# Kernel optimization log

Measured on AMD Instinct MI355X. Metric: run time of the kernel, lower is better.

Reference implementation:

```python
import jax, jax.numpy as jnp
import numpy as np

DIM = 256
N = 8192

def setup_inputs() -> dict:
    key = jax.random.key(0)
    kx, kq, kk, kv = jax.random.split(key, 4)
    X = jax.random.normal(kx, (N, DIM), dtype=jnp.float32)
    # nn.Linear weights are [out, in]; xavier-uniform-like scale via normal/sqrt(dim)
    Wq = jax.random.normal(kq, (DIM, DIM), dtype=jnp.float32) / np.sqrt(DIM)
    Wk = jax.random.normal(kk, (DIM, DIM), dtype=jnp.float32) / np.sqrt(DIM)
    Wv = jax.random.normal(kv, (DIM, DIM), dtype=jnp.float32) / np.sqrt(DIM)
    return {"X": X, "Wq": Wq, "Wk": Wk, "Wv": Wv}

def reference(X, Wq, Wk, Wv):
    # nn.Linear(no bias): y = X @ W.T
    Q = X @ Wq.T  # [N, D]
    K = X @ Wk.T
    V = X @ Wv.T
    scores = (Q @ K.T) / jnp.sqrt(jnp.asarray(DIM, dtype=X.dtype))  # [N, N]
    softed = jax.nn.softmax(scores, axis=-1)
    return softed @ V  # [N, D]
```

## Files before the change

### kernel.cpp

```cpp
#include <hip/hip_runtime.h>
#include <math.h>

#define N 8192
#define D 256
#define QBLK 128
#define KBLK 32

typedef float f32x4 __attribute__((ext_vector_type(4)));
typedef float f32x16 __attribute__((ext_vector_type(16)));
typedef short bf16x8 __attribute__((ext_vector_type(8)));

#define MFMA16(a, b, c) __builtin_amdgcn_mfma_f32_16x16x32_bf16((a), (b), (c), 0, 0, 0)
#define MFMA32(a, b, c) __builtin_amdgcn_mfma_f32_32x32x16_bf16((a), (b), (c), 0, 0, 0)
#define BAR() __builtin_amdgcn_s_barrier()
#define CFENCE() asm volatile("" ::: "memory")

__device__ __forceinline__ unsigned short f2b(float f) {
    unsigned u = __builtin_bit_cast(unsigned, f);
    u = u + 0x7fffu + ((u >> 16) & 1u);
    return (unsigned short)(u >> 16);
}
__device__ __forceinline__ unsigned pk2(float a, float b) {
    return (unsigned)f2b(a) | ((unsigned)f2b(b) << 16);
}
__device__ __forceinline__ unsigned cvtpk(float a, float b) {
    unsigned r;
    asm("v_cvt_pk_bf16_f32 %0, %1, %2" : "=v"(r) : "v"(a), "v"(b));
    return r;
}
__device__ __forceinline__ float b2f(short s) {
    unsigned x = ((unsigned)(unsigned short)s) << 16;
    return __builtin_bit_cast(float, x);
}

__global__ __launch_bounds__(256) void proj_mfma(
    const float* __restrict__ X, const float* __restrict__ Wq,
    const float* __restrict__ Wk, const float* __restrict__ Wv,
    unsigned short* __restrict__ Qb, unsigned short* __restrict__ Kb,
    unsigned short* __restrict__ Vt)
{
    __shared__ char Wl[32768];
    const int z = blockIdx.z;
    const float* W = (z == 0) ? Wq : (z == 1) ? Wk : Wv;
    const int r0 = blockIdx.x * 64;
    const int c0 = blockIdx.y * 64;
    const int t = threadIdx.x, w = t >> 6, l = t & 63;
    const int lo = l & 15, hi = l >> 4;

    #pragma unroll
    for (int i = 0; i < 16; ++i) {
        int e4 = t + i * 256;
        int col = e4 >> 6, kk4 = e4 & 63;
        float4 f = *(const float4*)&W[(size_t)(c0 + col) * D + kk4 * 4];
        unsigned long long v = (unsigned long long)pk2(f.x, f.y)
                             | ((unsigned long long)pk2(f.z, f.w) << 32);
        *(unsigned long long*)(Wl + col * 512 + ((kk4 * 8) ^ ((col & 7) << 4))) = v;
    }
    __syncthreads();

    bf16x8 xf[8];
    {
        const float* xr = X + (size_t)(r0 + w * 16 + lo) * D;
        #pragma unroll
        for (int ks = 0; ks < 8; ++ks) {
            float4 a = *(const float4*)(xr + ks * 32 + hi * 8);
            float4 b = *(const float4*)(xr + ks * 32 + hi * 8 + 4);
            bf16x8 v;
            v[0] = (short)f2b(a.x); v[1] = (short)f2b(a.y);
            v[2] = (short)f2b(a.z); v[3] = (short)f2b(a.w);
            v[4] = (short)f2b(b.x); v[5] = (short)f2b(b.y);
            v[6] = (short)f2b(b.z); v[7] = (short)f2b(b.w);
            xf[ks] = v;
        }
    }

    f32x4 acc[4];
    #pragma unroll
    for (int nc = 0; nc < 4; ++nc) acc[nc] = (f32x4){0.f, 0.f, 0.f, 0.f};
    #pragma unroll
    for (int ks = 0; ks < 8; ++ks) {
        #pragma unroll
        for (int nc = 0; nc < 4; ++nc) {
            int col = nc * 16 + lo;
            bf16x8 wf = *(const bf16x8*)(Wl + col * 512 +
                                         ((ks * 64 + hi * 16) ^ ((col & 7) << 4)));
            acc[nc] = MFMA16(xf[ks], wf, acc[nc]);
        }
    }

    if (z < 2) {
        unsigned short* Y = z ? Kb : Qb;
        #pragma unroll
        for (int nc = 0; nc < 4; ++nc)
            #pragma unroll
            for (int r = 0; r < 4; ++r)
                Y[(size_t)(r0 + w * 16 + hi * 4 + r) * D + c0 + nc * 16 + lo] = f2b(acc[nc][r]);
    } else {
        #pragma unroll
        for (int nc = 0; nc < 4; ++nc) {
            unsigned long long v = (unsigned long long)pk2(acc[nc][0], acc[nc][1])
                                 | ((unsigned long long)pk2(acc[nc][2], acc[nc][3]) << 32);
            *(unsigned long long*)&Vt[(size_t)(c0 + nc * 16 + lo) * N + r0 + w * 16 + hi * 4] = v;
        }
    }
}

__device__ __forceinline__ void stage_K(const unsigned short* __restrict__ Kb,
                                        char* kbuf, int kt, int t)
{
    #pragma unroll
    for (int i = 0; i < 4; ++i) {
        int c = t + i * 256;
        int r = c >> 5, xc = c & 31;
        int pk = (r & 0x13) | ((r & 4) << 1) | ((r & 8) >> 1);
        const unsigned short* gp = Kb + (size_t)(kt + pk) * D + (xc ^ (r & 7)) * 8;
        __builtin_amdgcn_global_load_lds(
            (const __attribute__((address_space(1))) void*)gp,
            (__attribute__((address_space(3))) void*)(kbuf + c * 16), 16, 0, 0);
    }
}
__device__ __forceinline__ void stage_V(const unsigned short* __restrict__ Vt,
                                        char* vbuf, int kt, int t)
{
    #pragma unroll
    for (int i = 0; i < 4; ++i) {
        int c = t + i * 256;
        int dd = c >> 2, xc = c & 3;
        const unsigned short* gp = Vt + (size_t)dd * N + kt + (xc ^ (dd & 3)) * 8;
        __builtin_amdgcn_global_load_lds(
            (const __attribute__((address_space(1))) void*)gp,
            (__attribute__((address_space(3))) void*)(vbuf + c * 16), 16, 0, 0);
    }
}

template <int KSPLIT>
__global__ __launch_bounds__(256, 2) void attn_mfma(
    const unsigned short* __restrict__ Qb,
    const unsigned short* __restrict__ Kb,
    const unsigned short* __restrict__ Vt,
    unsigned short* __restrict__ Opart,
    float2* __restrict__ ml)
{
    extern __shared__ char smem[];
    const int t = threadIdx.x;
    const int w = t >> 6;
    const int l = t & 63;
    const int r = l & 31;
    const int hi1 = l >> 5;
    const int bid = blockIdx.x;
    const int split = bid % KSPLIT;
    const int xblk = bid / KSPLIT;
    const int q0 = xblk * QBLK + w * 32;
    const int kbase = split * (N / KSPLIT);
    const int NTS = N / KSPLIT / KBLK;
    const int p0 = bid & (NTS - 1);

    bf16x8 qf[16];
    {
        const unsigned short* qrow = Qb + (size_t)(q0 + r) * D;
        #pragma unroll
        for (int ks = 0; ks < 16; ++ks)
            qf[ks] = *(const bf16x8*)(qrow + ks * 16 + hi1 * 8);
    }

    stage_K(Kb, smem,         kbase + p0 * KBLK, t);
    stage_V(Vt, smem + 32768, kbase + p0 * KBLK, t);
    stage_K(Kb, smem + 16384,         kbase + ((p0 + 1) & (NTS - 1)) * KBLK, t);
    stage_V(Vt, smem + 32768 + 16384, kbase + ((p0 + 1) & (NTS - 1)) * KBLK, t);

    f32x16 Oacc[8];
    #pragma unroll
    for (int nc = 0; nc < 8; ++nc)
        #pragma unroll
        for (int e = 0; e < 16; ++e) Oacc[nc][e] = 0.f;
    float m_run = -INFINITY, l_run = 0.f;
    const float scale2 = 0.09016994f;

    asm volatile("s_waitcnt vmcnt(8)" ::: "memory");
    BAR();

    for (int tt = 0; tt < NTS; ++tt) {
        const int cur = tt & 1;
        char* Kl = smem + cur * 16384;
        char* Vl = smem + 32768 + cur * 16384;

        f32x16 sacc;
        #pragma unroll
        for (int e = 0; e < 16; ++e) sacc[e] = 0.f;
        __builtin_amdgcn_s_setprio(1);
        #pragma unroll
        for (int ks = 0; ks < 16; ++ks) {
            bf16x8 kf = *(const bf16x8*)(Kl + r * 512 + (((ks * 2 + hi1) ^ (r & 7)) * 16));
            sacc = MFMA32(kf, qf[ks], sacc);
        }
        __builtin_amdgcn_s_setprio(0);

        if (tt + 2 < NTS) {
            CFENCE(); BAR(); CFENCE();
            stage_K(Kb, Kl, kbase + ((p0 + tt + 2) & (NTS - 1)) * KBLK, t);
        }

        float m0 = fmaxf(fmaxf(sacc[0], sacc[1]),   fmaxf(sacc[2], sacc[3]));
        float m1 = fmaxf(fmaxf(sacc[4], sacc[5]),   fmaxf(sacc[6], sacc[7]));
        float m2 = fmaxf(fmaxf(sacc[8], sacc[9]),   fmaxf(sacc[10], sacc[11]));
        float m3 = fmaxf(fmaxf(sacc[12], sacc[13]), fmaxf(sacc[14], sacc[15]));
        float pm = fmaxf(fmaxf(m0, m1), fmaxf(m2, m3)) * scale2;

        bool need = pm > m_run + 11.0f;
        if (__builtin_expect(__any(need), 0)) {
            float m2x = fmaxf(pm, __shfl_xor(pm, 32));
            float m_new = fmaxf(m_run, m2x);
            float corr = exp2f(m_run - m_new);
            m_run = m_new;
            l_run *= corr;
            #pragma unroll
            for (int nc = 0; nc < 8; ++nc)
                #pragma unroll
                for (int e = 0; e < 16; ++e) Oacc[nc][e] *= corr;
        }

        bf16x8 pb[2];
        float sum = 0.f;
        #pragma unroll
        for (int s1 = 0; s1 < 2; ++s1) {
            union { unsigned u[4]; bf16x8 v; } uu;
            #pragma unroll
            for (int j2 = 0; j2 < 4; ++j2) {
                float a = exp2f(sacc[s1 * 8 + j2 * 2]     * scale2 - m_run);
                float b = exp2f(sacc[s1 * 8 + j2 * 2 + 1] * scale2 - m_run);
                sum += a + b;
                uu.u[j2] = cvtpk(a, b);
            }
            pb[s1] = uu.v;
        }
        l_run += sum;

        __builtin_amdgcn_s_setprio(1);
        #pragma unroll
        for (int nc = 0; nc < 8; ++nc) {
            const char* vrow = Vl + (nc * 32 + r) * 64;
            bf16x8 va0 = *(const bf16x8*)(vrow + ((hi1       ^ (r & 3)) * 16));
            bf16x8 va1 = *(const bf16x8*)(vrow + (((2 + hi1) ^ (r & 3)) * 16));
            Oacc[nc] = MFMA32(va0, pb[0], Oacc[nc]);
            Oacc[nc] = MFMA32(va1, pb[1], Oacc[nc]);
        }
        __builtin_amdgcn_s_setprio(0);

        if (tt + 2 < NTS) {
            CFENCE(); BAR(); CFENCE();
            stage_V(Vt, Vl, kbase + ((p0 + tt + 2) & (NTS - 1)) * KBLK, t);
            asm volatile("s_waitcnt vmcnt(8)" ::: "memory");
            BAR(); CFENCE();
        } else if (tt + 1 < NTS) {
            asm volatile("s_waitcnt vmcnt(0)" ::: "memory");
            BAR(); CFENCE();
        }
    }

    l_run += __shfl_xor(l_run, 32);
    const size_t orow = ((size_t)split * N + q0 + r) * D;
    #pragma unroll
    for (int nc = 0; nc < 8; ++nc)
        #pragma unroll
        for (int g = 0; g < 4; ++g) {
            unsigned long long v =
                  (unsigned long long)pk2(Oacc[nc][g * 4 + 0], Oacc[nc][g * 4 + 1])
                | ((unsigned long long)pk2(Oacc[nc][g * 4 + 2], Oacc[nc][g * 4 + 3]) << 32);
            *(unsigned long long*)&Opart[orow + nc * 32 + g * 8 + hi1 * 4] = v;
        }
    if (l < 32)
        ml[(size_t)split * N + q0 + r] = make_float2(m_run, l_run);
}

__global__ __launch_bounds__(256) void combine_kernel(
    const unsigned short* __restrict__ Opart, const float2* __restrict__ ml,
    float* __restrict__ out, int nsplit)
{
    int idx = blockIdx.x * 256 + threadIdx.x;
    int q = idx >> 5;
    int d0 = (idx & 31) * 8;

    float M = -INFINITY;
    for (int i = 0; i < nsplit; ++i) M = fmaxf(M, ml[(size_t)i * N + q].x);
    float L = 0.f;
    float acc[8] = {};
    for (int i = 0; i < nsplit; ++i) {
        float2 v = ml[(size_t)i * N + q];
        float wgt = exp2f(v.x - M);
        L += wgt * v.y;
        bf16x8 ov = *(const bf16x8*)&Opart[((size_t)i * N + q) * D + d0];
        #pragma unroll
        for (int j = 0; j < 8; ++j) acc[j] += wgt * b2f(ov[j]);
    }
    float r = 1.f / L;
    #pragma unroll
    for (int j = 0; j < 8; ++j) out[(size_t)q * D + d0 + j] = acc[j] * r;
}

extern "C" void kernel_launch(void* const* d_in, const int* in_sizes, int n_in,
                              void* d_out, int out_size, void* d_ws, size_t ws_size,
                              hipStream_t stream) {
    const float* X  = (const float*)d_in[0];
    const float* Wq = (const float*)d_in[1];
    const float* Wk = (const float*)d_in[2];
    const float* Wv = (const float*)d_in[3];

    unsigned short* ws = (unsigned short*)d_ws;
    const size_t ndq = (size_t)N * D;
    unsigned short* Qb = ws;
    unsigned short* Kb = ws + ndq;
    unsigned short* Vt = ws + 2 * ndq;
    unsigned short* Opart = ws + 3 * ndq;

    auto need = [ndq](int ks) {
        return (size_t)(3 + ks) * ndq * 2 + (size_t)ks * N * 8;
    };
    const int ksplit = (ws_size >= need(8)) ? 8 : (ws_size >= need(4)) ? 4 : 2;
    float2* ml = (float2*)(ws + (3 + ksplit) * ndq);

    (void)hipFuncSetAttribute((const void*)attn_mfma<8>,
                              hipFuncAttributeMaxDynamicSharedMemorySize, 65536);
    (void)hipFuncSetAttribute((const void*)attn_mfma<4>,
                              hipFuncAttributeMaxDynamicSharedMemorySize, 65536);
    (void)hipFuncSetAttribute((const void*)attn_mfma<2>,
                              hipFuncAttributeMaxDynamicSharedMemorySize, 65536);

    proj_mfma<<<dim3(N / 64, D / 64, 3), 256, 0, stream>>>(X, Wq, Wk, Wv, Qb, Kb, Vt);
    if (ksplit == 8)
        attn_mfma<8><<<dim3((N / QBLK) * 8), 256, 65536, stream>>>(Qb, Kb, Vt, Opart, ml);
    else if (ksplit == 4)
        attn_mfma<4><<<dim3((N / QBLK) * 4), 256, 65536, stream>>>(Qb, Kb, Vt, Opart, ml);
    else
        attn_mfma<2><<<dim3((N / QBLK) * 2), 256, 65536, stream>>>(Qb, Kb, Vt, Opart, ml);
    combine_kernel<<<(N * D / 8) / 256, 256, 0, stream>>>(Opart, ml, (float*)d_out, ksplit);
}
```

Before: 127.7 us.

## Batch LDS fragment loads ahead of MFMA groups, precompute staging offsets, change V swizzle

```diff
diff --git a/kernel.cpp b/kernel.cpp
--- a/kernel.cpp
+++ b/kernel.cpp
@@ -102,34 +102,6 @@
                                  | ((unsigned long long)pk2(acc[nc][2], acc[nc][3]) << 32);
             *(unsigned long long*)&Vt[(size_t)(c0 + nc * 16 + lo) * N + r0 + w * 16 + hi * 4] = v;
         }
-    }
-}
-
-__device__ __forceinline__ void stage_K(const unsigned short* __restrict__ Kb,
-                                        char* kbuf, int kt, int t)
-{
-    #pragma unroll
-    for (int i = 0; i < 4; ++i) {
-        int c = t + i * 256;
-        int r = c >> 5, xc = c & 31;
-        int pk = (r & 0x13) | ((r & 4) << 1) | ((r & 8) >> 1);
-        const unsigned short* gp = Kb + (size_t)(kt + pk) * D + (xc ^ (r & 7)) * 8;
-        __builtin_amdgcn_global_load_lds(
-            (const __attribute__((address_space(1))) void*)gp,
-            (__attribute__((address_space(3))) void*)(kbuf + c * 16), 16, 0, 0);
-    }
-}
-__device__ __forceinline__ void stage_V(const unsigned short* __restrict__ Vt,
-                                        char* vbuf, int kt, int t)
-{
-    #pragma unroll
-    for (int i = 0; i < 4; ++i) {
-        int c = t + i * 256;
-        int dd = c >> 2, xc = c & 3;
-        const unsigned short* gp = Vt + (size_t)dd * N + kt + (xc ^ (dd & 3)) * 8;
-        __builtin_amdgcn_global_load_lds(
-            (const __attribute__((address_space(1))) void*)gp,
-            (__attribute__((address_space(3))) void*)(vbuf + c * 16), 16, 0, 0);
     }
 }
 
@@ -155,6 +127,34 @@
     const int NTS = N / KSPLIT / KBLK;
     const int p0 = bid & (NTS - 1);
 
+    unsigned ksoff[4], vsoff[4];
+    #pragma unroll
+    for (int i = 0; i < 4; ++i) {
+        int c = t + i * 256;
+        int rr = c >> 5, xc = c & 31;
+        int pk = (rr & 0x13) | ((rr & 4) << 1) | ((rr & 8) >> 1);
+        ksoff[i] = (unsigned)(pk * D + (xc ^ (rr & 7)) * 8);
+        int dd = c >> 2, x2 = c & 3;
+        vsoff[i] = (unsigned)(dd * N + (x2 ^ ((dd >> 1) & 3)) * 8);
+    }
+
+    auto stageK = [&](char* kbuf, int tile) {
+        const unsigned koff = (unsigned)(kbase + tile * KBLK) * D;
+        #pragma unroll
+        for (int i = 0; i < 4; ++i)
+            __builtin_amdgcn_global_load_lds(
+                (const __attribute__((address_space(1))) void*)(Kb + koff + ksoff[i]),
+                (__attribute__((address_space(3))) void*)(kbuf + (t + i * 256) * 16), 16, 0, 0);
+    };
+    auto stageV = [&](char* vbuf, int tile) {
+        const unsigned voff = (unsigned)(kbase + tile * KBLK);
+        #pragma unroll
+        for (int i = 0; i < 4; ++i)
+            __builtin_amdgcn_global_load_lds(
+                (const __attribute__((address_space(1))) void*)(Vt + voff + vsoff[i]),
+                (__attribute__((address_space(3))) void*)(vbuf + (t + i * 256) * 16), 16, 0, 0);
+    };
+
     bf16x8 qf[16];
     {
         const unsigned short* qrow = Qb + (size_t)(q0 + r) * D;
@@ -163,10 +163,10 @@
             qf[ks] = *(const bf16x8*)(qrow + ks * 16 + hi1 * 8);
     }
 
-    stage_K(Kb, smem,         kbase + p0 * KBLK, t);
-    stage_V(Vt, smem + 32768, kbase + p0 * KBLK, t);
-    stage_K(Kb, smem + 16384,         kbase + ((p0 + 1) & (NTS - 1)) * KBLK, t);
-    stage_V(Vt, smem + 32768 + 16384, kbase + ((p0 + 1) & (NTS - 1)) * KBLK, t);
+    stageK(smem, p0);
+    stageV(smem + 32768, p0);
+    stageK(smem + 16384, (p0 + 1) & (NTS - 1));
+    stageV(smem + 32768 + 16384, (p0 + 1) & (NTS - 1));
 
     f32x16 Oacc[8];
     #pragma unroll
@@ -187,17 +187,30 @@
         f32x16 sacc;
         #pragma unroll
         for (int e = 0; e < 16; ++e) sacc[e] = 0.f;
+
+        bf16x8 kf8[8];
+        #pragma unroll
+        for (int j = 0; j < 8; ++j)
+            kf8[j] = *(const bf16x8*)(Kl + r * 512 + (((j * 2 + hi1) ^ (r & 7)) * 16));
         __builtin_amdgcn_s_setprio(1);
         #pragma unroll
-        for (int ks = 0; ks < 16; ++ks) {
-            bf16x8 kf = *(const bf16x8*)(Kl + r * 512 + (((ks * 2 + hi1) ^ (r & 7)) * 16));
-            sacc = MFMA32(kf, qf[ks], sacc);
-        }
+        for (int j = 0; j < 8; ++j)
+            sacc = MFMA32(kf8[j], qf[j], sacc);
+        __builtin_amdgcn_s_setprio(0);
+
+        bf16x8 kg8[8];
+        #pragma unroll
+        for (int j = 0; j < 8; ++j)
+            kg8[j] = *(const bf16x8*)(Kl + r * 512 + ((((8 + j) * 2 + hi1) ^ (r & 7)) * 16));
+        __builtin_amdgcn_s_setprio(1);
+        #pragma unroll
+        for (int j = 0; j < 8; ++j)
+            sacc = MFMA32(kg8[j], qf[8 + j], sacc);
         __builtin_amdgcn_s_setprio(0);
 
         if (tt + 2 < NTS) {
             CFENCE(); BAR(); CFENCE();
-            stage_K(Kb, Kl, kbase + ((p0 + tt + 2) & (NTS - 1)) * KBLK, t);
+            stageK(Kl, (p0 + tt + 2) & (NTS - 1));
         }
 
         float m0 = fmaxf(fmaxf(sacc[0], sacc[1]),   fmaxf(sacc[2], sacc[3]));
@@ -226,8 +239,8 @@
             union { unsigned u[4]; bf16x8 v; } uu;
             #pragma unroll
             for (int j2 = 0; j2 < 4; ++j2) {
-                float a = exp2f(sacc[s1 * 8 + j2 * 2]     * scale2 - m_run);
-                float b = exp2f(sacc[s1 * 8 + j2 * 2 + 1] * scale2 - m_run);
+                float a = __builtin_amdgcn_exp2f(sacc[s1 * 8 + j2 * 2]     * scale2 - m_run);
+                float b = __builtin_amdgcn_exp2f(sacc[s1 * 8 + j2 * 2 + 1] * scale2 - m_run);
                 sum += a + b;
                 uu.u[j2] = cvtpk(a, b);
             }
@@ -235,20 +248,39 @@
         }
         l_run += sum;
 
+        bf16x8 vf8[8];
+        #pragma unroll
+        for (int nc = 0; nc < 4; ++nc) {
+            const char* vrow = Vl + (nc * 32 + r) * 64;
+            vf8[nc * 2 + 0] = *(const bf16x8*)(vrow + (((0 + hi1) ^ ((r >> 1) & 3)) * 16));
+            vf8[nc * 2 + 1] = *(const bf16x8*)(vrow + (((2 + hi1) ^ ((r >> 1) & 3)) * 16));
+        }
         __builtin_amdgcn_s_setprio(1);
         #pragma unroll
-        for (int nc = 0; nc < 8; ++nc) {
-            const char* vrow = Vl + (nc * 32 + r) * 64;
-            bf16x8 va0 = *(const bf16x8*)(vrow + ((hi1       ^ (r & 3)) * 16));
-            bf16x8 va1 = *(const bf16x8*)(vrow + (((2 + hi1) ^ (r & 3)) * 16));
-            Oacc[nc] = MFMA32(va0, pb[0], Oacc[nc]);
-            Oacc[nc] = MFMA32(va1, pb[1], Oacc[nc]);
+        for (int nc = 0; nc < 4; ++nc) {
+            Oacc[nc] = MFMA32(vf8[nc * 2 + 0], pb[0], Oacc[nc]);
+            Oacc[nc] = MFMA32(vf8[nc * 2 + 1], pb[1], Oacc[nc]);
+        }
+        __builtin_amdgcn_s_setprio(0);
+
+        bf16x8 vg8[8];
+        #pragma unroll
+        for (int nc = 0; nc < 4; ++nc) {
+            const char* vrow = Vl + ((nc + 4) * 32 + r) * 64;
+            vg8[nc * 2 + 0] = *(const bf16x8*)(vrow + (((0 + hi1) ^ ((r >> 1) & 3)) * 16));
+            vg8[nc * 2 + 1] = *(const bf16x8*)(vrow + (((2 + hi1) ^ ((r >> 1) & 3)) * 16));
+        }
+        __builtin_amdgcn_s_setprio(1);
+        #pragma unroll
+        for (int nc = 0; nc < 4; ++nc) {
+            Oacc[nc + 4] = MFMA32(vg8[nc * 2 + 0], pb[0], Oacc[nc + 4]);
+            Oacc[nc + 4] = MFMA32(vg8[nc * 2 + 1], pb[1], Oacc[nc + 4]);
         }
         __builtin_amdgcn_s_setprio(0);
 
         if (tt + 2 < NTS) {
             CFENCE(); BAR(); CFENCE();
-            stage_V(Vt, Vl, kbase + ((p0 + tt + 2) & (NTS - 1)) * KBLK, t);
+            stageV(Vl, (p0 + tt + 2) & (NTS - 1));
             asm volatile("s_waitcnt vmcnt(8)" ::: "memory");
             BAR(); CFENCE();
         } else if (tt + 1 < NTS) {
```

Result: no change. 125.6 us (-1.7%).
